# Performance work log

Hardware: AMD Instinct MI355X
Metric: run time of the kernel (lower is better)

## Reference

```python
import jax, jax.numpy as jnp
import numpy as np

NUM_HEADS = 4

def setup_inputs() -> dict:
    key = jax.random.key(0)
    ks = jax.random.split(key, 5)
    B, N, C = 2, 4096, 256
    s = 0.02
    return {
        "x": jax.random.normal(ks[0], (B, N, C), dtype=jnp.float32),
        "qkv_w": jax.random.normal(ks[1], (3 * C, C), dtype=jnp.float32) * s,
        "qkv_b": jax.random.normal(ks[2], (3 * C,), dtype=jnp.float32) * s,
        "out_w": jax.random.normal(ks[3], (C, C), dtype=jnp.float32) * s,
        "out_b": jax.random.normal(ks[4], (C,), dtype=jnp.float32) * s,
    }

def reference(x, qkv_w, qkv_b, out_w, out_b):
    # x: [B, N, C]; manual multi-head self-attention (eval mode, dropout off)
    B, N, C = x.shape
    H = NUM_HEADS
    D = C // H
    qkv = x @ qkv_w.T + qkv_b                      # [B, N, 3C]
    qkv = qkv.reshape(B, N, 3, H, D)
    qkv = jnp.transpose(qkv, (2, 0, 3, 1, 4))      # [3, B, H, N, D]
    q, k, v = qkv[0], qkv[1], qkv[2]
    scale = D ** -0.5
    attn = jnp.einsum('bhnd,bhmd->bhnm', q, k) * scale  # [B, H, N, N]
    attn = jax.nn.softmax(attn, axis=-1)
    out = jnp.einsum('bhnm,bhmd->bhnd', attn, v)   # [B, H, N, D]
    out = jnp.transpose(out, (0, 2, 1, 3)).reshape(B, N, C)
    return out @ out_w.T + out_b
```

## Files before the change

kernel.cpp:

```cpp
#include <hip/hip_runtime.h>

typedef __bf16 bf16x8 __attribute__((ext_vector_type(8)));
typedef float f32x4 __attribute__((ext_vector_type(4)));

#define MFMA_BF16(a, b, c) __builtin_amdgcn_mfma_f32_16x16x32_bf16((a), (b), (c), 0, 0, 0)

#define C1 0.18033688f

static __device__ __forceinline__ unsigned short f2bf(float f) {
    unsigned int u = __float_as_uint(f);
    unsigned int r = (u + 0x7fffu + ((u >> 16) & 1u)) >> 16;
    return (unsigned short)r;
}
static __device__ __forceinline__ float bf2f(unsigned short us) {
    return __uint_as_float(((unsigned int)us) << 16);
}
static __device__ __forceinline__ float exp2_hw(float x) {
    float r;
    asm("v_exp_f32 %0, %1" : "=v"(r) : "v"(x));
    return r;
}
static __device__ __forceinline__ unsigned pack_rh(float a, float b) {
    return __byte_perm(__float_as_uint(a) + 0x8000u, __float_as_uint(b) + 0x8000u, 0x7632);
}
static __device__ __forceinline__ void gload16(const void* g, void* l) {
    __builtin_amdgcn_global_load_lds(
        (const __attribute__((address_space(1))) unsigned int*)g,
        (__attribute__((address_space(3))) unsigned int*)l, 16, 0, 0);
}

static __device__ __forceinline__ void conv_seg8(const void* src, unsigned short* dst, int n,
                                                 int lb, bool f32) {
    const int base = lb * 2048 + (int)threadIdx.x * 8;
    if (base < n) {
        if (f32) {
            const float4 u0 = *(const float4*)((const float*)src + base);
            const float4 u1 = *(const float4*)((const float*)src + base + 4);
            uint4 p;
            p.x = pack_rh(u0.x, u0.y);
            p.y = pack_rh(u0.z, u0.w);
            p.z = pack_rh(u1.x, u1.y);
            p.w = pack_rh(u1.z, u1.w);
            *(uint4*)(dst + base) = p;
        } else {
            *(uint4*)(dst + base) = *(const uint4*)((const unsigned short*)src + base);
        }
    }
}

__global__ __launch_bounds__(256) void convert_kernel(
    const void* __restrict__ x, const void* __restrict__ qw, const void* __restrict__ qb,
    const void* __restrict__ ow, const void* __restrict__ ob,
    unsigned short* __restrict__ xb, unsigned short* __restrict__ qwb,
    unsigned short* __restrict__ qbb, unsigned short* __restrict__ owb,
    unsigned short* __restrict__ obb, int* __restrict__ flag) {
    __shared__ int tot;
    if (threadIdx.x == 0) tot = 0;
    __syncthreads();
    {
        unsigned short v = ((const unsigned short*)x)[threadIdx.x];
        int e = (v >> 7) & 0xFF;
        if (e >= 195) atomicAdd(&tot, 1);
    }
    __syncthreads();
    const bool f32 = (tot >= 8);
    if (blockIdx.x == 0 && threadIdx.x == 0) flag[0] = f32 ? 1 : 0;

    const int bid = blockIdx.x;
    if (bid < 1024)       conv_seg8(x,  xb,  2097152, bid,        f32);
    else if (bid < 1120)  conv_seg8(qw, qwb, 196608,  bid - 1024, f32);
    else if (bid < 1121)  conv_seg8(qb, qbb, 768,     bid - 1120, f32);
    else if (bid < 1153)  conv_seg8(ow, owb, 65536,   bid - 1121, f32);
    else                  conv_seg8(ob, obb, 256,     bid - 1153, f32);
}

template <bool QKV>
__global__ __launch_bounds__(256) void gemm_kernel(
    const unsigned short* __restrict__ A, const unsigned short* __restrict__ W,
    const unsigned short* __restrict__ bias, unsigned short* __restrict__ Cb,
    float* __restrict__ Cf, const int* __restrict__ flag,
    unsigned short* __restrict__ Vt, int Nout) {
    constexpr int K = 256;
    __shared__ __align__(16) char sm[16384];

    const int tid = threadIdx.x;
    const int lane = tid & 63;
    const int wv = tid >> 6;
    const int m16 = lane & 15;
    const int quad = lane >> 4;
    const int bm = blockIdx.x * 64;
    const int bn = blockIdx.y * 64;

    int bgo[2], blo[2];
#pragma unroll
    for (int i = 0; i < 2; i++) {
        const int c = wv * 128 + i * 64 + lane;
        const int r = c >> 3, g = (c & 7) ^ (r & 7);
        bgo[i] = r * (K * 2) + g * 16;
        blo[i] = c * 16;
    }
    int bro[4][2];
#pragma unroll
    for (int t = 0; t < 4; t++)
#pragma unroll
        for (int ks = 0; ks < 2; ks++) {
            const int row = t * 16 + m16;
            bro[t][ks] = row * 64 + ((4 * ks + quad) ^ (m16 & 7)) * 8;
        }

    const char* bg = (const char*)(W + (size_t)bn * K);
    const unsigned short* ap = A + (size_t)(bm + wv * 16 + m16) * K + quad * 8;

#pragma unroll
    for (int i = 0; i < 2; i++) gload16(bg + bgo[i], sm + blo[i]);
    bf16x8 a0 = *(const bf16x8*)(ap);
    bf16x8 a1 = *(const bf16x8*)(ap + 32);

    f32x4 acc[4] = {};
#pragma unroll
    for (int kb = 0; kb < 4; kb++) {
        __syncthreads();
        const int cur = kb & 1;
        bf16x8 a0n, a1n;
        if (kb < 3) {
            bg += 128;
            char* Bdst = sm + (cur ^ 1) * 8192;
#pragma unroll
            for (int i = 0; i < 2; i++) gload16(bg + bgo[i], Bdst + blo[i]);
            a0n = *(const bf16x8*)(ap + (kb + 1) * 64);
            a1n = *(const bf16x8*)(ap + (kb + 1) * 64 + 32);
        }
        const unsigned short* Blds = (const unsigned short*)(sm + cur * 8192);
#pragma unroll
        for (int ks = 0; ks < 2; ks++) {
            const bf16x8 a = ks ? a1 : a0;
#pragma unroll
            for (int t = 0; t < 4; t++) {
                const bf16x8 b = *(const bf16x8*)(Blds + bro[t][ks]);
                acc[t] = MFMA_BF16(a, b, acc[t]);
            }
        }
        if (kb < 3) {
            a0 = a0n;
            a1 = a1n;
        }
    }

    if (QKV && bn >= 512) {
        __syncthreads();
        unsigned short* tr = (unsigned short*)sm;
        const int lr = wv * 16 + quad * 4;
#pragma unroll
        for (int t = 0; t < 4; t++) {
            const float bv = bf2f(bias[bn + t * 16 + m16]);
            uint2 w;
            w.x = pack_rh(acc[t][0] + bv, acc[t][1] + bv);
            w.y = pack_rh(acc[t][2] + bv, acc[t][3] + bv);
            *(uint2*)&tr[(t * 16 + m16) * 72 + lr] = w;
        }
        __syncthreads();
        const int d = tid >> 2;
        const int ch = (tid & 3) * 16;
        const uint4 o4a = *(const uint4*)&tr[d * 72 + ch];
        const uint4 o4b = *(const uint4*)&tr[d * 72 + ch + 8];
        const int hh = (bn - 512) >> 6;
        const int bb = bm >> 12, n0 = bm & 4095;
        unsigned short* vdst = &Vt[((size_t)((bb * 4 + hh) * 64 + d)) * 4096 + n0 + ch];
        *(uint4*)(vdst) = o4a;
        *(uint4*)(vdst + 8) = o4b;
        return;
    }

    const bool outf = (!QKV) && (flag != nullptr) && (*flag != 0);
    const int row0 = bm + wv * 16 + quad * 4;
#pragma unroll
    for (int t = 0; t < 4; t++) {
        const int col = bn + t * 16 + m16;
        const float bv = bf2f(bias[col]);
        float v[4];
#pragma unroll
        for (int r = 0; r < 4; r++) v[r] = acc[t][r] + bv;
        if (QKV) {
            const float sc = (col < 256) ? C1 : 1.0f;
#pragma unroll
            for (int r = 0; r < 4; r++)
                Cb[(size_t)(row0 + r) * 768 + col] = f2bf(v[r] * sc);
        } else {
            if (outf) {
#pragma unroll
                for (int r = 0; r < 4; r++) Cf[(size_t)(row0 + r) * Nout + col] = v[r];
            } else {
#pragma unroll
                for (int r = 0; r < 4; r++) Cb[(size_t)(row0 + r) * Nout + col] = f2bf(v[r]);
            }
        }
    }
}

__global__ __launch_bounds__(256) void attn_kernel(
    const unsigned short* __restrict__ qkv, const unsigned short* __restrict__ Vt,
    unsigned short* __restrict__ attn, int iters) {
    const int N = 4096, C3 = 768;
    __shared__ __align__(16) char sm[65536];

    const int tid = threadIdx.x;
    const int lane = tid & 63;
    const int wv = tid >> 6;
    const int m16 = lane & 15;
    const int quad = lane >> 4;

    const int bh = blockIdx.x & 7;
    const int qt = blockIdx.x >> 3;
    const int b = bh >> 2, h = bh & 3;

    bf16x8 qf[4][2];
#pragma unroll
    for (int j = 0; j < 4; j++)
#pragma unroll
        for (int ks = 0; ks < 2; ks++)
            qf[j][ks] = *(const bf16x8*)(qkv + ((size_t)b * N + qt * 64 + j * 16 + m16) * C3 +
                                         h * 64 + ks * 32 + quad * 8);

    uint4 ones_u;
    ones_u.x = ones_u.y = ones_u.z = ones_u.w = 0x3F803F80u;
    const bf16x8 ones = *(const bf16x8*)&ones_u;

    int kgo[4], vgo[4], klo[4], vlo[4];
#pragma unroll
    for (int i = 0; i < 4; i++) {
        const int c = wv * 256 + i * 64 + lane;
        const int r = c >> 3, g = (c & 7) ^ (r & 7);
        kgo[i] = r * 1536 + g * 16;
        klo[i] = c * 16;
        const int d = c >> 4, gg = (c & 15) ^ (d & 15);
        vgo[i] = d * 8192 + gg * 16;
        vlo[i] = c * 16;
    }
    int kro[2][2], vro[4], pwo[2][4], pro[4];
#pragma unroll
    for (int mb = 0; mb < 2; mb++)
#pragma unroll
        for (int ks = 0; ks < 2; ks++) {
            const int row = wv * 32 + mb * 16 + m16;
            kro[mb][ks] = row * 64 + ((4 * ks + quad) ^ (m16 & 7)) * 8;
        }
#pragma unroll
    for (int t = 0; t < 4; t++) vro[t] = (t * 16 + m16) * 128 + ((wv * 4 + quad) ^ m16) * 8;
#pragma unroll
    for (int mb = 0; mb < 2; mb++)
#pragma unroll
        for (int j = 0; j < 4; j++)
            pwo[mb][j] = wv * 2048 + (j * 16 + m16) * 32 +
                         ((2 * mb + (quad >> 1)) ^ (m16 & 3)) * 8 + (quad & 1) * 4;
#pragma unroll
    for (int j = 0; j < 4; j++)
        pro[j] = wv * 2048 + (j * 16 + m16) * 32 + (quad ^ (m16 & 3)) * 8;

    const char* kgp = (const char*)(qkv + (size_t)b * N * C3 + 256 + h * 64);
    const char* vgp = (const char*)(Vt + (size_t)bh * 64 * N);

#pragma unroll
    for (int i = 0; i < 4; i++) {
        gload16(kgp + kgo[i], sm + klo[i]);
        gload16(vgp + vgo[i], sm + 32768 + vlo[i]);
    }

    f32x4 o[4][4] = {};
    f32x4 o1[4] = {};

    for (int kt = 0; kt < iters; ++kt) {
        __syncthreads();
        const int cur = kt & 1;
        if (kt + 1 < iters) {
            kgp += 128 * 1536;
            vgp += 256;
            char* Kdst = sm + (cur ^ 1) * 16384;
            char* Vdst = sm + 32768 + (cur ^ 1) * 16384;
#pragma unroll
            for (int i = 0; i < 4; i++) {
                gload16(kgp + kgo[i], Kdst + klo[i]);
                gload16(vgp + vgo[i], Vdst + vlo[i]);
            }
        }
        unsigned short* Kb = (unsigned short*)(sm + cur * 16384);
        const unsigned short* Vb = (const unsigned short*)(sm + 32768 + cur * 16384);

        f32x4 s[2][4] = {};
#pragma unroll
        for (int mb = 0; mb < 2; mb++)
#pragma unroll
            for (int ks = 0; ks < 2; ks++) {
                const bf16x8 ka = *(const bf16x8*)(Kb + kro[mb][ks]);
#pragma unroll
                for (int j = 0; j < 4; j++) s[mb][j] = MFMA_BF16(ka, qf[j][ks], s[mb][j]);
            }

#pragma unroll
        for (int mb = 0; mb < 2; mb++)
#pragma unroll
            for (int j = 0; j < 4; j++) {
                const float p0 = exp2_hw(s[mb][j][0]);
                const float p1 = exp2_hw(s[mb][j][1]);
                const float p2 = exp2_hw(s[mb][j][2]);
                const float p3 = exp2_hw(s[mb][j][3]);
                uint2 w;
                w.x = pack_rh(p0, p1);
                w.y = pack_rh(p2, p3);
                *(uint2*)(Kb + pwo[mb][j]) = w;
            }
        asm volatile("s_waitcnt lgkmcnt(0)" ::: "memory");

        bf16x8 pa[4];
#pragma unroll
        for (int j = 0; j < 4; j++) pa[j] = *(const bf16x8*)(Kb + pro[j]);
#pragma unroll
        for (int j = 0; j < 4; j++) o1[j] = MFMA_BF16(pa[j], ones, o1[j]);
#pragma unroll
        for (int t = 0; t < 4; t++) {
            const bf16x8 vb = *(const bf16x8*)(Vb + vro[t]);
#pragma unroll
            for (int j = 0; j < 4; j++) o[j][t] = MFMA_BF16(pa[j], vb, o[j][t]);
        }
    }

    __syncthreads();
    float* Ored = (float*)sm;
    float* lsum = (float*)(sm + 16384);
    if (m16 == 0) {
#pragma unroll
        for (int j = 0; j < 4; j++)
#pragma unroll
            for (int r = 0; r < 4; r++)
                lsum[wv * 64 + j * 16 + quad * 4 + r] = o1[j][r];
    }
    const int row = tid >> 4;
    const int col = (tid & 15) * 4;
#pragma unroll
    for (int j = 0; j < 4; j++) {
#pragma unroll
        for (int t = 0; t < 4; t++)
#pragma unroll
            for (int r = 0; r < 4; r++)
                Ored[(wv * 16 + quad * 4 + r) * 64 + t * 16 + m16] = o[j][t][r];
        __syncthreads();
        f32x4 sum = *(f32x4*)&Ored[row * 64 + col];
        sum += *(f32x4*)&Ored[1024 + row * 64 + col];
        sum += *(f32x4*)&Ored[2048 + row * 64 + col];
        sum += *(f32x4*)&Ored[3072 + row * 64 + col];
        const float lq = lsum[j * 16 + row] + lsum[64 + j * 16 + row] +
                         lsum[128 + j * 16 + row] + lsum[192 + j * 16 + row];
        const int n = qt * 64 + j * 16 + row;
        const float inv = 1.0f / lq;
        uint2 w;
        w.x = pack_rh(sum[0] * inv, sum[1] * inv);
        w.y = pack_rh(sum[2] * inv, sum[3] * inv);
        *(uint2*)&attn[((size_t)b * N + n) * 256 + h * 64 + col] = w;
        __syncthreads();
    }
}

extern "C" void kernel_launch(void* const* d_in, const int* in_sizes, int n_in,
                              void* d_out, int out_size, void* d_ws, size_t ws_size,
                              hipStream_t stream) {
    const int B = 2, N = 4096, H = 4;
    const int M = B * N;

    char* wsb = (char*)d_ws;
    int* flag = (int*)wsb;
    unsigned short* xb      = (unsigned short*)(wsb + 64);
    unsigned short* qwb     = xb + 2097152;
    unsigned short* qbb     = qwb + 196608;
    unsigned short* owb     = qbb + 768;
    unsigned short* obb     = owb + 65536;
    unsigned short* qkv_ws  = obb + 256;
    unsigned short* Vt_ws   = qkv_ws + 6291456;
    unsigned short* attn_ws = Vt_ws + 2097152;

    convert_kernel<<<1154, 256, 0, stream>>>(d_in[0], d_in[1], d_in[2], d_in[3], d_in[4],
                                             xb, qwb, qbb, owb, obb, flag);

    gemm_kernel<true><<<dim3(M / 64, 768 / 64), 256, 0, stream>>>(
        xb, qwb, qbb, qkv_ws, nullptr, nullptr, Vt_ws, 768);

    attn_kernel<<<512, 256, 0, stream>>>(qkv_ws, Vt_ws, attn_ws, 32);

    gemm_kernel<false><<<dim3(M / 64, 256 / 64), 256, 0, stream>>>(
        attn_ws, owb, obb, (unsigned short*)d_out, (float*)d_out, flag, nullptr, 256);
}
```

Before: 144.8 us.

## Split attention work across eight waves by query and key groups

The attention kernel moves from 4 to 8 waves per block. Each wave now owns 16 query rows and half of each 128-key tile, instead of 4 waves each handling 32 keys for all 64 queries. Probabilities go to a separate per-wave LDS scratch rather than overwriting the K tile, and the epilogue reduces only two partial results per row instead of four. The aim is more waves in flight and fewer accumulator registers per thread, at the cost of more LDS per block (72KB) and a smaller share of K/V loads per thread.

```diff
diff --git a/kernel.cpp b/kernel.cpp
--- a/kernel.cpp
+++ b/kernel.cpp
@@ -197,38 +197,38 @@
     }
 }
 
-__global__ __launch_bounds__(256) void attn_kernel(
+__global__ __launch_bounds__(512, 4) void attn_kernel(
     const unsigned short* __restrict__ qkv, const unsigned short* __restrict__ Vt,
     unsigned short* __restrict__ attn, int iters) {
     const int N = 4096, C3 = 768;
-    __shared__ __align__(16) char sm[65536];
+    __shared__ __align__(16) char sm[73728];
 
     const int tid = threadIdx.x;
     const int lane = tid & 63;
     const int wv = tid >> 6;
     const int m16 = lane & 15;
     const int quad = lane >> 4;
+    const int qg = wv >> 1;
+    const int kg = wv & 1;
 
     const int bh = blockIdx.x & 7;
     const int qt = blockIdx.x >> 3;
     const int b = bh >> 2, h = bh & 3;
 
-    bf16x8 qf[4][2];
-#pragma unroll
-    for (int j = 0; j < 4; j++)
-#pragma unroll
-        for (int ks = 0; ks < 2; ks++)
-            qf[j][ks] = *(const bf16x8*)(qkv + ((size_t)b * N + qt * 64 + j * 16 + m16) * C3 +
-                                         h * 64 + ks * 32 + quad * 8);
+    bf16x8 qf[2];
+#pragma unroll
+    for (int ks = 0; ks < 2; ks++)
+        qf[ks] = *(const bf16x8*)(qkv + ((size_t)b * N + qt * 64 + qg * 16 + m16) * C3 +
+                                  h * 64 + ks * 32 + quad * 8);
 
     uint4 ones_u;
     ones_u.x = ones_u.y = ones_u.z = ones_u.w = 0x3F803F80u;
     const bf16x8 ones = *(const bf16x8*)&ones_u;
 
-    int kgo[4], vgo[4], klo[4], vlo[4];
-#pragma unroll
-    for (int i = 0; i < 4; i++) {
-        const int c = wv * 256 + i * 64 + lane;
+    int kgo[2], klo[2], vgo[2], vlo[2];
+#pragma unroll
+    for (int i = 0; i < 2; i++) {
+        const int c = wv * 128 + i * 64 + lane;
         const int r = c >> 3, g = (c & 7) ^ (r & 7);
         kgo[i] = r * 1536 + g * 16;
         klo[i] = c * 16;
@@ -236,37 +236,37 @@
         vgo[i] = d * 8192 + gg * 16;
         vlo[i] = c * 16;
     }
-    int kro[2][2], vro[4], pwo[2][4], pro[4];
-#pragma unroll
-    for (int mb = 0; mb < 2; mb++)
+    int kro[4][2], vro[4][2];
+#pragma unroll
+    for (int kb = 0; kb < 4; kb++)
 #pragma unroll
         for (int ks = 0; ks < 2; ks++) {
-            const int row = wv * 32 + mb * 16 + m16;
-            kro[mb][ks] = row * 64 + ((4 * ks + quad) ^ (m16 & 7)) * 8;
-        }
-#pragma unroll
-    for (int t = 0; t < 4; t++) vro[t] = (t * 16 + m16) * 128 + ((wv * 4 + quad) ^ m16) * 8;
-#pragma unroll
-    for (int mb = 0; mb < 2; mb++)
-#pragma unroll
-        for (int j = 0; j < 4; j++)
-            pwo[mb][j] = wv * 2048 + (j * 16 + m16) * 32 +
-                         ((2 * mb + (quad >> 1)) ^ (m16 & 3)) * 8 + (quad & 1) * 4;
-#pragma unroll
-    for (int j = 0; j < 4; j++)
-        pro[j] = wv * 2048 + (j * 16 + m16) * 32 + (quad ^ (m16 & 3)) * 8;
+            const int row = kg * 64 + kb * 16 + m16;
+            kro[kb][ks] = row * 64 + ((4 * ks + quad) ^ (m16 & 7)) * 8;
+        }
+#pragma unroll
+    for (int t = 0; t < 4; t++)
+#pragma unroll
+        for (int h2 = 0; h2 < 2; h2++)
+            vro[t][h2] = (t * 16 + m16) * 128 + ((kg * 8 + h2 * 4 + quad) ^ m16) * 8;
+    unsigned short* P = (unsigned short*)(sm + 65536) + wv * 512;
+    int pwo[2];
+#pragma unroll
+    for (int kb2 = 0; kb2 < 2; kb2++)
+        pwo[kb2] = m16 * 32 + ((kb2 * 2 + (quad >> 1)) ^ (m16 & 3)) * 8 + (quad & 1) * 4;
+    const int pro = m16 * 32 + (quad ^ (m16 & 3)) * 8;
 
     const char* kgp = (const char*)(qkv + (size_t)b * N * C3 + 256 + h * 64);
     const char* vgp = (const char*)(Vt + (size_t)bh * 64 * N);
 
 #pragma unroll
-    for (int i = 0; i < 4; i++) {
+    for (int i = 0; i < 2; i++) {
         gload16(kgp + kgo[i], sm + klo[i]);
         gload16(vgp + vgo[i], sm + 32768 + vlo[i]);
     }
 
-    f32x4 o[4][4] = {};
-    f32x4 o1[4] = {};
+    f32x4 o[4] = {};
+    f32x4 o1 = {};
 
     for (int kt = 0; kt < iters; ++kt) {
         __syncthreads();
@@ -277,85 +277,89 @@
             char* Kdst = sm + (cur ^ 1) * 16384;
             char* Vdst = sm + 32768 + (cur ^ 1) * 16384;
 #pragma unroll
-            for (int i = 0; i < 4; i++) {
+            for (int i = 0; i < 2; i++) {
                 gload16(kgp + kgo[i], Kdst + klo[i]);
                 gload16(vgp + vgo[i], Vdst + vlo[i]);
             }
         }
-        unsigned short* Kb = (unsigned short*)(sm + cur * 16384);
+        const unsigned short* Kb = (const unsigned short*)(sm + cur * 16384);
         const unsigned short* Vb = (const unsigned short*)(sm + 32768 + cur * 16384);
 
-        f32x4 s[2][4] = {};
-#pragma unroll
-        for (int mb = 0; mb < 2; mb++)
+        f32x4 s[4] = {};
+#pragma unroll
+        for (int kb = 0; kb < 4; kb++)
 #pragma unroll
             for (int ks = 0; ks < 2; ks++) {
-                const bf16x8 ka = *(const bf16x8*)(Kb + kro[mb][ks]);
-#pragma unroll
-                for (int j = 0; j < 4; j++) s[mb][j] = MFMA_BF16(ka, qf[j][ks], s[mb][j]);
-            }
-
-#pragma unroll
-        for (int mb = 0; mb < 2; mb++)
-#pragma unroll
-            for (int j = 0; j < 4; j++) {
-                const float p0 = exp2_hw(s[mb][j][0]);
-                const float p1 = exp2_hw(s[mb][j][1]);
-                const float p2 = exp2_hw(s[mb][j][2]);
-                const float p3 = exp2_hw(s[mb][j][3]);
+                const bf16x8 ka = *(const bf16x8*)(Kb + kro[kb][ks]);
+                s[kb] = MFMA_BF16(ka, qf[ks], s[kb]);
+            }
+
+#pragma unroll
+        for (int h2 = 0; h2 < 2; h2++) {
+#pragma unroll
+            for (int kb2 = 0; kb2 < 2; kb2++) {
+                const int kb = h2 * 2 + kb2;
+                const float p0 = exp2_hw(s[kb][0]);
+                const float p1 = exp2_hw(s[kb][1]);
+                const float p2 = exp2_hw(s[kb][2]);
+                const float p3 = exp2_hw(s[kb][3]);
                 uint2 w;
                 w.x = pack_rh(p0, p1);
                 w.y = pack_rh(p2, p3);
-                *(uint2*)(Kb + pwo[mb][j]) = w;
-            }
-        asm volatile("s_waitcnt lgkmcnt(0)" ::: "memory");
-
-        bf16x8 pa[4];
-#pragma unroll
-        for (int j = 0; j < 4; j++) pa[j] = *(const bf16x8*)(Kb + pro[j]);
-#pragma unroll
-        for (int j = 0; j < 4; j++) o1[j] = MFMA_BF16(pa[j], ones, o1[j]);
-#pragma unroll
-        for (int t = 0; t < 4; t++) {
-            const bf16x8 vb = *(const bf16x8*)(Vb + vro[t]);
-#pragma unroll
-            for (int j = 0; j < 4; j++) o[j][t] = MFMA_BF16(pa[j], vb, o[j][t]);
+                *(uint2*)(P + pwo[kb2]) = w;
+            }
+            asm volatile("s_waitcnt lgkmcnt(0)" ::: "memory");
+            const bf16x8 pa = *(const bf16x8*)(P + pro);
+            o1 = MFMA_BF16(pa, ones, o1);
+#pragma unroll
+            for (int t = 0; t < 4; t++) {
+                const bf16x8 vb = *(const bf16x8*)(Vb + vro[t][h2]);
+                o[t] = MFMA_BF16(pa, vb, o[t]);
+            }
         }
     }
 
     __syncthreads();
     float* Ored = (float*)sm;
-    float* lsum = (float*)(sm + 16384);
-    if (m16 == 0) {
-#pragma unroll
-        for (int j = 0; j < 4; j++)
+    float* lsum = (float*)(sm + 65536);
+    const int qrow0 = qg * 16 + quad * 4;
+    if (kg == 1) {
+#pragma unroll
+        for (int t = 0; t < 4; t++)
 #pragma unroll
             for (int r = 0; r < 4; r++)
-                lsum[wv * 64 + j * 16 + quad * 4 + r] = o1[j][r];
-    }
-    const int row = tid >> 4;
-    const int col = (tid & 15) * 4;
-#pragma unroll
-    for (int j = 0; j < 4; j++) {
+                Ored[(qrow0 + r) * 68 + t * 16 + m16] = o[t][r];
+        if (m16 == 0) {
+#pragma unroll
+            for (int r = 0; r < 4; r++) lsum[qrow0 + r] = o1[r];
+        }
+    }
+    __syncthreads();
+    if (kg == 0) {
+        float inv[4];
+#pragma unroll
+        for (int r = 0; r < 4; r++) inv[r] = 1.0f / (o1[r] + lsum[qrow0 + r]);
 #pragma unroll
         for (int t = 0; t < 4; t++)
 #pragma unroll
-            for (int r = 0; r < 4; r++)
-                Ored[(wv * 16 + quad * 4 + r) * 64 + t * 16 + m16] = o[j][t][r];
-        __syncthreads();
-        f32x4 sum = *(f32x4*)&Ored[row * 64 + col];
-        sum += *(f32x4*)&Ored[1024 + row * 64 + col];
-        sum += *(f32x4*)&Ored[2048 + row * 64 + col];
-        sum += *(f32x4*)&Ored[3072 + row * 64 + col];
-        const float lq = lsum[j * 16 + row] + lsum[64 + j * 16 + row] +
-                         lsum[128 + j * 16 + row] + lsum[192 + j * 16 + row];
-        const int n = qt * 64 + j * 16 + row;
-        const float inv = 1.0f / lq;
-        uint2 w;
-        w.x = pack_rh(sum[0] * inv, sum[1] * inv);
-        w.y = pack_rh(sum[2] * inv, sum[3] * inv);
-        *(uint2*)&attn[((size_t)b * N + n) * 256 + h * 64 + col] = w;
-        __syncthreads();
+            for (int r = 0; r < 4; r++) {
+                const int idx = (qrow0 + r) * 68 + t * 16 + m16;
+                Ored[idx] = (o[t][r] + Ored[idx]) * inv[r];
+            }
+    }
+    __syncthreads();
+    {
+        const int q64 = tid >> 3;
+        const int dch = (tid & 7) * 8;
+        const float* src = &Ored[q64 * 68 + dch];
+        const f32x4 v0 = *(const f32x4*)(src);
+        const f32x4 v1 = *(const f32x4*)(src + 4);
+        uint4 w;
+        w.x = pack_rh(v0[0], v0[1]);
+        w.y = pack_rh(v0[2], v0[3]);
+        w.z = pack_rh(v1[0], v1[1]);
+        w.w = pack_rh(v1[2], v1[3]);
+        *(uint4*)&attn[((size_t)b * N + qt * 64 + q64) * 256 + h * 64 + dch] = w;
     }
 }
 
@@ -382,7 +386,7 @@
     gemm_kernel<true><<<dim3(M / 64, 768 / 64), 256, 0, stream>>>(
         xb, qwb, qbb, qkv_ws, nullptr, nullptr, Vt_ws, 768);
 
-    attn_kernel<<<512, 256, 0, stream>>>(qkv_ws, Vt_ws, attn_ws, 32);
+    attn_kernel<<<512, 512, 0, stream>>>(qkv_ws, Vt_ws, attn_ws, 32);
 
     gemm_kernel<false><<<dim3(M / 64, 256 / 64), 256, 0, stream>>>(
         attn_ws, owb, obb, (unsigned short*)d_out, (float*)d_out, flag, nullptr, 256);
```

Result: no change. 145.3 us (+0.3%).

## Keep softmax probabilities in registers instead of round-tripping through LDS

Applied to the files above, without the earlier changes.

The exponentiated score fragments are packed straight into the MFMA A-operand registers rather than written to shared memory and read back. The V reads are remapped into two 8-byte LDS loads so that their k-index ordering matches the register-resident probability layout. This removes an LDS write, a wait on lgkmcnt and an LDS read per iteration. In exchange it doubles the number of V loads, and it relies on the permuted k ordering being consistent between P and V.

```diff
diff --git a/kernel.cpp b/kernel.cpp
--- a/kernel.cpp
+++ b/kernel.cpp
@@ -236,7 +236,7 @@
         vgo[i] = d * 8192 + gg * 16;
         vlo[i] = c * 16;
     }
-    int kro[2][2], vro[4], pwo[2][4], pro[4];
+    int kro[2][2];
 #pragma unroll
     for (int mb = 0; mb < 2; mb++)
 #pragma unroll
@@ -244,17 +244,10 @@
             const int row = wv * 32 + mb * 16 + m16;
             kro[mb][ks] = row * 64 + ((4 * ks + quad) ^ (m16 & 7)) * 8;
         }
-#pragma unroll
-    for (int t = 0; t < 4; t++) vro[t] = (t * 16 + m16) * 128 + ((wv * 4 + quad) ^ m16) * 8;
-#pragma unroll
-    for (int mb = 0; mb < 2; mb++)
-#pragma unroll
-        for (int j = 0; j < 4; j++)
-            pwo[mb][j] = wv * 2048 + (j * 16 + m16) * 32 +
-                         ((2 * mb + (quad >> 1)) ^ (m16 & 3)) * 8 + (quad & 1) * 4;
-#pragma unroll
-    for (int j = 0; j < 4; j++)
-        pro[j] = wv * 2048 + (j * 16 + m16) * 32 + (quad ^ (m16 & 3)) * 8;
+    int vroA[4];
+#pragma unroll
+    for (int t = 0; t < 4; t++)
+        vroA[t] = (t * 16 + m16) * 128 + (((wv * 4 + (quad >> 1)) ^ m16) * 8) + (quad & 1) * 4;
 
     const char* kgp = (const char*)(qkv + (size_t)b * N * C3 + 256 + h * 64);
     const char* vgp = (const char*)(Vt + (size_t)bh * 64 * N);
@@ -282,7 +275,7 @@
                 gload16(vgp + vgo[i], Vdst + vlo[i]);
             }
         }
-        unsigned short* Kb = (unsigned short*)(sm + cur * 16384);
+        const unsigned short* Kb = (const unsigned short*)(sm + cur * 16384);
         const unsigned short* Vb = (const unsigned short*)(sm + 32768 + cur * 16384);
 
         f32x4 s[2][4] = {};
@@ -295,29 +288,37 @@
                 for (int j = 0; j < 4; j++) s[mb][j] = MFMA_BF16(ka, qf[j][ks], s[mb][j]);
             }
 
-#pragma unroll
-        for (int mb = 0; mb < 2; mb++)
-#pragma unroll
-            for (int j = 0; j < 4; j++) {
-                const float p0 = exp2_hw(s[mb][j][0]);
-                const float p1 = exp2_hw(s[mb][j][1]);
-                const float p2 = exp2_hw(s[mb][j][2]);
-                const float p3 = exp2_hw(s[mb][j][3]);
-                uint2 w;
-                w.x = pack_rh(p0, p1);
-                w.y = pack_rh(p2, p3);
-                *(uint2*)(Kb + pwo[mb][j]) = w;
-            }
-        asm volatile("s_waitcnt lgkmcnt(0)" ::: "memory");
-
         bf16x8 pa[4];
 #pragma unroll
-        for (int j = 0; j < 4; j++) pa[j] = *(const bf16x8*)(Kb + pro[j]);
+        for (int j = 0; j < 4; j++) {
+            const float e0 = exp2_hw(s[0][j][0]);
+            const float e1 = exp2_hw(s[0][j][1]);
+            const float e2 = exp2_hw(s[0][j][2]);
+            const float e3 = exp2_hw(s[0][j][3]);
+            const float e4 = exp2_hw(s[1][j][0]);
+            const float e5 = exp2_hw(s[1][j][1]);
+            const float e6 = exp2_hw(s[1][j][2]);
+            const float e7 = exp2_hw(s[1][j][3]);
+            uint4 pw;
+            pw.x = pack_rh(e0, e1);
+            pw.y = pack_rh(e2, e3);
+            pw.z = pack_rh(e4, e5);
+            pw.w = pack_rh(e6, e7);
+            pa[j] = *(const bf16x8*)&pw;
+        }
+
 #pragma unroll
         for (int j = 0; j < 4; j++) o1[j] = MFMA_BF16(pa[j], ones, o1[j]);
 #pragma unroll
         for (int t = 0; t < 4; t++) {
-            const bf16x8 vb = *(const bf16x8*)(Vb + vro[t]);
+            const uint2 va = *(const uint2*)(Vb + vroA[t]);
+            const uint2 vc = *(const uint2*)(Vb + (vroA[t] ^ 16));
+            uint4 vv;
+            vv.x = va.x;
+            vv.y = va.y;
+            vv.z = vc.x;
+            vv.w = vc.y;
+            const bf16x8 vb = *(const bf16x8*)&vv;
 #pragma unroll
             for (int j = 0; j < 4; j++) o[j][t] = MFMA_BF16(pa[j], vb, o[j][t]);
         }
```

Result: no change. 142.3 us (-1.8%).
